# Performance work log

Hardware: AMD Instinct MI355X
Metric: run time of the kernel (lower is better)

Reference implementation:

```python
import jax, jax.numpy as jnp
import numpy as np

L = 50000          # n_agents - 1 neighbors
OBS = 256          # input_shape[0]
ACT = 64           # output_shape
OTHER = 512        # input_shape[1]
HID = 64           # rnn_hidden_dim (forced by attn shape: 64 + cate_dim)
CATE = 32          # cate_dim


def setup_inputs() -> dict:
    key = jax.random.key(0)
    ks = jax.random.split(key, 16)
    s = 0.05
    return {
        "inputs": jax.random.normal(ks[0], (OBS,), jnp.float32),
        "act_idx": jax.random.normal(ks[1], (ACT,), jnp.float32),
        "other_inputs": jax.random.normal(ks[2], (L, OTHER), jnp.float32),
        # fc11: Linear(OBS+ACT, 64)
        "W11": jax.random.normal(ks[3], (HID, OBS + ACT), jnp.float32) * s,
        "b11": jax.random.normal(ks[4], (HID,), jnp.float32) * s,
        # fc12: Linear(OTHER, CATE)
        "W12": jax.random.normal(ks[5], (CATE, OTHER), jnp.float32) * s,
        "b12": jax.random.normal(ks[6], (CATE,), jnp.float32) * s,
        # attn: Linear(HID+CATE, 1)
        "Wa": jax.random.normal(ks[7], (1, HID + CATE), jnp.float32) * s,
        "ba": jax.random.normal(ks[8], (1,), jnp.float32) * s,
        # attn_out: Linear(CATE, CATE)
        "Wao": jax.random.normal(ks[9], (CATE, CATE), jnp.float32) * s,
        "bao": jax.random.normal(ks[10], (CATE,), jnp.float32) * s,
        # fc2: Linear(HID+CATE, HID)
        "W2": jax.random.normal(ks[11], (HID, HID + CATE), jnp.float32) * s,
        "b2": jax.random.normal(ks[12], (HID,), jnp.float32) * s,
        # fc3: Linear(HID, 1)
        "W3": jax.random.normal(ks[13], (1, HID), jnp.float32) * s,
        "b3": jax.random.normal(ks[14], (1,), jnp.float32) * s,
    }


def reference(inputs, act_idx, other_inputs, W11, b11, W12, b12, Wa, ba, Wao, bao, W2, b2, W3, b3):
    # cat obs with one-hot-style action index vector (dim 0 of 1D tensors)
    x_in = jnp.concatenate([inputs, act_idx])            # [OBS+ACT]
    input_x = W11 @ x_in + b11                           # [HID]

    # per-neighbor embedding (vectorized over the L neighbors)
    emb = other_inputs @ W12.T + b12                     # [L, CATE]

    # attention score attn(relu(cat(input_x, emb_i))); relu is elementwise,
    # so split the attn weight into the input_x part and the emb part.
    rx = jax.nn.relu(input_x)                            # [HID]
    re = jax.nn.relu(emb)                                # [L, CATE]
    w = rx @ Wa[0, :HID] + re @ Wa[0, HID:] + ba[0]      # [L]
    aw = jax.nn.softmax(w)                               # softmax over neighbors

    # attention-weighted mixture of neighbor embeddings
    mixed = aw @ emb                                     # [CATE]
    mixed = jax.nn.relu(mixed) @ Wao.T + bao             # attn_out

    # straight-through categorical (argmax one-hot, soft gradient)
    z_prob = jax.nn.softmax(mixed)                       # [CATE]
    samples = jax.nn.one_hot(jnp.argmax(z_prob), CATE, dtype=z_prob.dtype)
    one_hot_st = samples + (z_prob - jax.lax.stop_gradient(z_prob))

    x = jax.nn.relu(jnp.concatenate([input_x, one_hot_st]))  # [HID+CATE]
    h = jax.nn.relu(W2 @ x + b2)                             # [HID]
    r = W3 @ h + b3                                          # [1]
    return (r, samples)
```

## Files before the change

### kernel.cpp

```cpp
#include <hip/hip_runtime.h>

#define L_N    50000
#define K_DIM  512
#define GRID1  256
#define NGRP   3125
#define SB()   __builtin_amdgcn_sched_barrier(0)

typedef __attribute__((ext_vector_type(8))) short bf16x8;
typedef __attribute__((ext_vector_type(4))) float f32x4;

__device__ __forceinline__ void split8(float4 a, float4 b, bf16x8& hi, bf16x8& lo) {
    float v[8] = {a.x, a.y, a.z, a.w, b.x, b.y, b.z, b.w};
    #pragma unroll
    for (int j = 0; j < 8; ++j) {
        unsigned u  = __float_as_uint(v[j]);
        unsigned hb = u & 0xFFFF0000u;
        float    lf = v[j] - __uint_as_float(hb);
        hi[j] = (short)(hb >> 16);
        lo[j] = (short)(__float_as_uint(lf) >> 16);
    }
}

__global__ __launch_bounds__(1024) void k_part(
    const float* __restrict__ other,
    const float* __restrict__ W12,
    const float* __restrict__ b12,
    const float* __restrict__ Wa,
    float* __restrict__ ws)
{
    __shared__ short whi[16384];
    __shared__ short wlo[16384];
    __shared__ float sbuf[16][34];

    const int tid  = threadIdx.x;
    const int lane = tid & 63;
    const int wv   = tid >> 6;
    const int cl   = lane & 15;
    const int g    = lane >> 4;

    #pragma unroll
    for (int c2 = 0; c2 < 2; ++c2) {
        const int u  = tid + c2 * 1024;
        const int ch = u >> 6, r = u & 63;
        const float* wp = W12 + (size_t)ch * K_DIM + (r >> 2) * 32 + (r & 3) * 4;
        const float4 f0 = *(const float4*)wp;
        const float4 f1 = *(const float4*)(wp + 16);
        bf16x8 h8, l8; split8(f0, f1, h8, l8);
        const int p = (r * 32 + (ch ^ (r & 31))) * 8;
        *(bf16x8*)&whi[p] = h8;
        *(bf16x8*)&wlo[p] = l8;
    }
    __syncthreads();

    float rps = 0.f, rm0 = 0.f, rm1 = 0.f;
    const int wid = blockIdx.x * 16 + wv;

    if (wid < NGRP) {
        const float b0 = b12[cl],     b1 = b12[16 + cl];
        const float w0 = Wa[64 + cl], w1 = Wa[80 + cl];

        const float* xp = other + (size_t)(wid * 16 + cl) * K_DIM + (g << 2);
        float4 Q0[4], Q1[4];

        #define ISSUE4(dst, q) do {                                            \
            _Pragma("unroll")                                                  \
            for (int i = 0; i < 4; ++i)                                        \
                dst[i] = *(const float4*)(xp + (q) * 64 + (i >> 1) * 32 + (i & 1) * 16); \
        } while (0)

        f32x4 acc0 = {0.f,0.f,0.f,0.f}, acc1 = {0.f,0.f,0.f,0.f};

        #define CONSUME4(buf, q) do {                                          \
            _Pragma("unroll")                                                  \
            for (int kk = 0; kk < 2; ++kk) {                                   \
                const int kc = (q) * 2 + kk;                                   \
                bf16x8 ah, al; split8(buf[kk * 2], buf[kk * 2 + 1], ah, al);   \
                const int r  = kc * 4 + g;                                     \
                const int u0 = (r * 32 + (cl ^ (r & 31))) * 8;                 \
                const bf16x8 bh0 = *(const bf16x8*)&whi[u0];                   \
                const bf16x8 bl0 = *(const bf16x8*)&wlo[u0];                   \
                const bf16x8 bh1 = *(const bf16x8*)&whi[u0 ^ 128];             \
                const bf16x8 bl1 = *(const bf16x8*)&wlo[u0 ^ 128];             \
                acc0 = __builtin_amdgcn_mfma_f32_16x16x32_bf16(ah, bh0, acc0, 0, 0, 0); \
                acc0 = __builtin_amdgcn_mfma_f32_16x16x32_bf16(al, bh0, acc0, 0, 0, 0); \
                acc0 = __builtin_amdgcn_mfma_f32_16x16x32_bf16(ah, bl0, acc0, 0, 0, 0); \
                acc1 = __builtin_amdgcn_mfma_f32_16x16x32_bf16(ah, bh1, acc1, 0, 0, 0); \
                acc1 = __builtin_amdgcn_mfma_f32_16x16x32_bf16(al, bh1, acc1, 0, 0, 0); \
                acc1 = __builtin_amdgcn_mfma_f32_16x16x32_bf16(ah, bl1, acc1, 0, 0, 0); \
            }                                                                  \
        } while (0)

        ISSUE4(Q0, 0); SB();
        ISSUE4(Q1, 1); SB();
        CONSUME4(Q0, 0); ISSUE4(Q0, 2); SB();
        CONSUME4(Q1, 1); ISSUE4(Q1, 3); SB();
        CONSUME4(Q0, 2); ISSUE4(Q0, 4); SB();
        CONSUME4(Q1, 3); ISSUE4(Q1, 5); SB();
        CONSUME4(Q0, 4); ISSUE4(Q0, 6); SB();
        CONSUME4(Q1, 5); ISSUE4(Q1, 7); SB();
        CONSUME4(Q0, 6);
        CONSUME4(Q1, 7);

        float e0[4], e1[4], s4[4];
        #pragma unroll
        for (int i = 0; i < 4; ++i) {
            e0[i] = acc0[i] + b0;
            e1[i] = acc1[i] + b1;
            s4[i] = fmaxf(e0[i], 0.f) * w0 + fmaxf(e1[i], 0.f) * w1;
        }
        #pragma unroll
        for (int d = 1; d < 16; d <<= 1) {
            #pragma unroll
            for (int i = 0; i < 4; ++i) s4[i] += __shfl_xor(s4[i], d);
        }
        #pragma unroll
        for (int i = 0; i < 4; ++i) {
            const float p = __expf(s4[i]);
            rps += p;
            rm0 = fmaf(p, e0[i], rm0);
            rm1 = fmaf(p, e1[i], rm1);
        }
    }

    rps += __shfl_xor(rps, 16); rps += __shfl_xor(rps, 32);
    rm0 += __shfl_xor(rm0, 16); rm0 += __shfl_xor(rm0, 32);
    rm1 += __shfl_xor(rm1, 16); rm1 += __shfl_xor(rm1, 32);
    if (lane == 0)  sbuf[wv][0] = rps;
    if (lane < 16) { sbuf[wv][1 + cl] = rm0; sbuf[wv][17 + cl] = rm1; }
    __syncthreads();
    if (wv == 0 && lane < 33) {
        float v = 0.f;
        #pragma unroll
        for (int s = 0; s < 16; ++s) v += sbuf[s][lane];
        ws[lane * GRID1 + blockIdx.x] = v;
    }
}

__global__ __launch_bounds__(256) void k_final(
    const float* __restrict__ ws,
    const float* __restrict__ inputs,
    const float* __restrict__ act_idx,
    const float* __restrict__ W11, const float* __restrict__ b11,
    const float* __restrict__ Wao, const float* __restrict__ bao,
    const float* __restrict__ W2,  const float* __restrict__ b2,
    const float* __restrict__ W3,  const float* __restrict__ b3,
    float* __restrict__ out)
{
    __shared__ float xsin[320];
    __shared__ float wsl[33];
    __shared__ float rm[32], z[32], xcat[96], h64[64];
    __shared__ int   amax;

    const int t = threadIdx.x, hh = t >> 2, q = t & 3;

    if (t < 132) {
        const int c = t >> 2, seg = t & 3;
        const float4* p = (const float4*)(ws + c * GRID1 + seg * 64);
        float v = 0.f;
        #pragma unroll
        for (int i = 0; i < 16; ++i) { const float4 f = p[i]; v += f.x + f.y + f.z + f.w; }
        v += __shfl_xor(v, 1);
        v += __shfl_xor(v, 2);
        if (seg == 0) wsl[c] = v;
    }
    xsin[t] = inputs[t];
    if (t < 64) xsin[256 + t] = act_idx[t];
    __syncthreads();

    if (t < 32) rm[t] = fmaxf(wsl[1 + t] / wsl[0], 0.f);

    float bp = 0.f;
    {
        const float4* wrow = (const float4*)(W11 + hh * 320 + q * 80);
        #pragma unroll
        for (int i = 0; i < 20; ++i) {
            const float4 f = wrow[i];
            const int k = q * 80 + i * 4;
            bp = fmaf(f.x, xsin[k], bp);
            bp = fmaf(f.y, xsin[k + 1], bp);
            bp = fmaf(f.z, xsin[k + 2], bp);
            bp = fmaf(f.w, xsin[k + 3], bp);
        }
    }
    bp += __shfl_xor(bp, 1);
    bp += __shfl_xor(bp, 2);
    __syncthreads();

    if (t < 32) {
        float zz = bao[t];
        for (int d = 0; d < 32; ++d) zz = fmaf(Wao[t * 32 + d], rm[d], zz);
        z[t] = zz;
    }
    __syncthreads();
    if (t == 0) {
        int bi = 0; float bv = z[0];
        for (int c = 1; c < 32; ++c) { if (z[c] > bv) { bv = z[c]; bi = c; } }
        amax = bi;
    }
    __syncthreads();
    if (q == 0) xcat[hh] = fmaxf(bp + b11[hh], 0.f);
    if (t < 32) xcat[64 + t] = (t == amax) ? 1.f : 0.f;
    __syncthreads();

    float dp = 0.f;
    for (int i = 0; i < 24; ++i) {
        const int k = q * 24 + i;
        dp = fmaf(W2[hh * 96 + k], xcat[k], dp);
    }
    dp += __shfl_xor(dp, 1);
    dp += __shfl_xor(dp, 2);
    if (q == 0) h64[hh] = fmaxf(dp + b2[hh], 0.f);
    __syncthreads();

    if (t == 0) {
        float r = b3[0];
        for (int i = 0; i < 64; ++i) r = fmaf(W3[i], h64[i], r);
        out[0] = r;
    }
    if (t < 32) out[1 + t] = (t == amax) ? 1.f : 0.f;
}

extern "C" void kernel_launch(void* const* d_in, const int* in_sizes, int n_in,
                              void* d_out, int out_size, void* d_ws, size_t ws_size,
                              hipStream_t stream) {
    const float* inputs  = (const float*)d_in[0];
    const float* act_idx = (const float*)d_in[1];
    const float* other   = (const float*)d_in[2];
    const float* W11     = (const float*)d_in[3];
    const float* b11     = (const float*)d_in[4];
    const float* W12     = (const float*)d_in[5];
    const float* b12     = (const float*)d_in[6];
    const float* Wa      = (const float*)d_in[7];
    const float* Wao     = (const float*)d_in[9];
    const float* bao     = (const float*)d_in[10];
    const float* W2      = (const float*)d_in[11];
    const float* b2      = (const float*)d_in[12];
    const float* W3      = (const float*)d_in[13];
    const float* b3      = (const float*)d_in[14];
    float* ws = (float*)d_ws;

    k_part<<<GRID1, 1024, 0, stream>>>(other, W12, b12, Wa, ws);
    k_final<<<1, 256, 0, stream>>>(ws, inputs, act_idx, W11, b11,
                                   Wao, bao, W2, b2, W3, b3, (float*)d_out);
}
```

Before: 32.45 us.

## Fuse final reduction into main kernel via last-block-done atomic counter

```diff
diff --git a/kernel.cpp b/kernel.cpp
--- a/kernel.cpp
+++ b/kernel.cpp
@@ -4,6 +4,7 @@
 #define K_DIM  512
 #define GRID1  256
 #define NGRP   3125
+#define NSLOT  64
 #define SB()   __builtin_amdgcn_sched_barrier(0)
 
 typedef __attribute__((ext_vector_type(8))) short bf16x8;
@@ -21,16 +22,24 @@
     }
 }
 
-__global__ __launch_bounds__(1024) void k_part(
+__global__ __launch_bounds__(1024) void k_fused(
     const float* __restrict__ other,
     const float* __restrict__ W12,
     const float* __restrict__ b12,
     const float* __restrict__ Wa,
-    float* __restrict__ ws)
+    const float* __restrict__ inputs,
+    const float* __restrict__ act_idx,
+    const float* __restrict__ W11, const float* __restrict__ b11,
+    const float* __restrict__ Wao, const float* __restrict__ bao,
+    const float* __restrict__ W2,  const float* __restrict__ b2,
+    const float* __restrict__ W3,  const float* __restrict__ b3,
+    float* __restrict__ ws,
+    float* __restrict__ out)
 {
     __shared__ short whi[16384];
     __shared__ short wlo[16384];
     __shared__ float sbuf[16][34];
+    __shared__ int   elect;
 
     const int tid  = threadIdx.x;
     const int lane = tid & 63;
@@ -132,45 +141,41 @@
         float v = 0.f;
         #pragma unroll
         for (int s = 0; s < 16; ++s) v += sbuf[s][lane];
-        ws[lane * GRID1 + blockIdx.x] = v;
-    }
-}
-
-__global__ __launch_bounds__(256) void k_final(
-    const float* __restrict__ ws,
-    const float* __restrict__ inputs,
-    const float* __restrict__ act_idx,
-    const float* __restrict__ W11, const float* __restrict__ b11,
-    const float* __restrict__ Wao, const float* __restrict__ bao,
-    const float* __restrict__ W2,  const float* __restrict__ b2,
-    const float* __restrict__ W3,  const float* __restrict__ b3,
-    float* __restrict__ out)
-{
+        atomicAdd(ws + lane * NSLOT + (blockIdx.x & (NSLOT - 1)), v);
+        __threadfence();
+    }
+    __syncthreads();
+    if (tid == 0) {
+        const int v = __hip_atomic_fetch_add((int*)(ws + 33 * NSLOT), 1,
+                                             __ATOMIC_ACQ_REL, __HIP_MEMORY_SCOPE_AGENT);
+        elect = (v == GRID1 - 1);
+    }
+    __syncthreads();
+    if (!elect) return;
+
     __shared__ float xsin[320];
     __shared__ float wsl[33];
     __shared__ float rm[32], z[32], xcat[96], h64[64];
     __shared__ int   amax;
 
-    const int t = threadIdx.x, hh = t >> 2, q = t & 3;
-
+    const int t = tid, hh = t >> 2, q = t & 3;
     if (t < 132) {
         const int c = t >> 2, seg = t & 3;
-        const float4* p = (const float4*)(ws + c * GRID1 + seg * 64);
         float v = 0.f;
         #pragma unroll
-        for (int i = 0; i < 16; ++i) { const float4 f = p[i]; v += f.x + f.y + f.z + f.w; }
+        for (int i = 0; i < 16; ++i) v += atomicAdd(ws + c * NSLOT + seg * 16 + i, 0.f);
         v += __shfl_xor(v, 1);
         v += __shfl_xor(v, 2);
         if (seg == 0) wsl[c] = v;
     }
-    xsin[t] = inputs[t];
-    if (t < 64) xsin[256 + t] = act_idx[t];
+    if (t < 256) xsin[t] = inputs[t];
+    if (t < 64)  xsin[256 + t] = act_idx[t];
     __syncthreads();
 
     if (t < 32) rm[t] = fmaxf(wsl[1 + t] / wsl[0], 0.f);
 
     float bp = 0.f;
-    {
+    if (t < 256) {
         const float4* wrow = (const float4*)(W11 + hh * 320 + q * 80);
         #pragma unroll
         for (int i = 0; i < 20; ++i) {
@@ -181,9 +186,9 @@
             bp = fmaf(f.z, xsin[k + 2], bp);
             bp = fmaf(f.w, xsin[k + 3], bp);
         }
-    }
-    bp += __shfl_xor(bp, 1);
-    bp += __shfl_xor(bp, 2);
+        bp += __shfl_xor(bp, 1);
+        bp += __shfl_xor(bp, 2);
+    }
     __syncthreads();
 
     if (t < 32) {
@@ -198,18 +203,20 @@
         amax = bi;
     }
     __syncthreads();
-    if (q == 0) xcat[hh] = fmaxf(bp + b11[hh], 0.f);
+    if (t < 256 && q == 0) xcat[hh] = fmaxf(bp + b11[hh], 0.f);
     if (t < 32) xcat[64 + t] = (t == amax) ? 1.f : 0.f;
     __syncthreads();
 
     float dp = 0.f;
-    for (int i = 0; i < 24; ++i) {
-        const int k = q * 24 + i;
-        dp = fmaf(W2[hh * 96 + k], xcat[k], dp);
-    }
-    dp += __shfl_xor(dp, 1);
-    dp += __shfl_xor(dp, 2);
-    if (q == 0) h64[hh] = fmaxf(dp + b2[hh], 0.f);
+    if (t < 256) {
+        for (int i = 0; i < 24; ++i) {
+            const int k = q * 24 + i;
+            dp = fmaf(W2[hh * 96 + k], xcat[k], dp);
+        }
+        dp += __shfl_xor(dp, 1);
+        dp += __shfl_xor(dp, 2);
+        if (q == 0) h64[hh] = fmaxf(dp + b2[hh], 0.f);
+    }
     __syncthreads();
 
     if (t == 0) {
@@ -239,7 +246,9 @@
     const float* b3      = (const float*)d_in[14];
     float* ws = (float*)d_ws;
 
-    k_part<<<GRID1, 1024, 0, stream>>>(other, W12, b12, Wa, ws);
-    k_final<<<1, 256, 0, stream>>>(ws, inputs, act_idx, W11, b11,
-                                   Wao, bao, W2, b2, W3, b3, (float*)d_out);
+    hipMemsetAsync(ws, 0, (33 * NSLOT + 1) * sizeof(float), stream);
+    k_fused<<<GRID1, 1024, 0, stream>>>(other, W12, b12, Wa,
+                                        inputs, act_idx, W11, b11,
+                                        Wao, bao, W2, b2, W3, b3,
+                                        ws, (float*)d_out);
 }
```

New measurement: 46.91 us. 1.45x slower.
